# Performance work log

Measured on AMD Instinct MI355X. Metric: run time of the kernel, lower is better.

## Reference

```python
import jax, jax.numpy as jnp
import numpy as np

D = 64   # combine_doc_emb_len
H = 2    # heads
B = 256
S = 1024
SIDE = 56  # uid 32 + os 8 + zip 16

def _prelu(x, a):
    return jnp.where(x >= 0, x, a * x)

def _l2norm(x):
    n = jnp.sqrt(jnp.sum(x * x, axis=-1, keepdims=True))
    return x / jnp.maximum(n, 1e-12)

def _attn_branch(x_trans, y_trans, side, w1, b1, a1, w2, b2):
    b, s = x_trans.shape[0], x_trans.shape[1]
    xh = x_trans.reshape(b, s, H, D).transpose(0, 2, 1, 3)   # [B,H,S,D]
    yh = y_trans.reshape(b, 1, H, D).transpose(0, 2, 1, 3)   # [B,H,1,D]
    yhb = jnp.broadcast_to(yh, (b, H, s, D))
    sideb = jnp.broadcast_to(side[:, None, None, :], (b, H, s, side.shape[-1]))
    feat = jnp.concatenate([xh, xh * yhb, xh - yhb, yhb, sideb], axis=-1)  # [B,H,S,4D+SIDE]
    h1 = _prelu(feat @ w1 + b1, a1)          # [B,H,S,40]
    p = (h1 @ w2 + b2)[..., 0]               # [B,H,S]
    out = jnp.einsum('bhsd,bhs->bhd', xh, p).reshape(b, H * D)
    return p, out

def setup_inputs():
    key = jax.random.key(0)
    k = jax.random.split(key, 20)
    def n(i, shape, sc=1.0):
        return sc * jax.random.normal(k[i], shape, dtype=jnp.float32)
    return {
        'local_x_embs': n(0, (B, S, D)),
        'nonlocal_x_embs': n(1, (B, S, D)),
        'y_embs': n(2, (B, D)),
        'user_id_embs': n(3, (B, 32)),
        'os_embs': n(4, (B, 8)),
        'zip_code_embs': n(5, (B, 16)),
        'w_ty': n(6, (D, H * D), 0.05), 'b_ty': n(7, (H * D,), 0.05), 'a_ty': jnp.float32(0.25),
        'w_lx': n(8, (D, H * D), 0.05), 'b_lx': n(9, (H * D,), 0.05), 'a_lx': jnp.float32(0.25),
        'w_nx': n(10, (D, H * D), 0.05), 'b_nx': n(11, (H * D,), 0.05), 'a_nx': jnp.float32(0.25),
        'lw1': n(12, (4 * D + SIDE, 40), 0.05), 'lb1': n(13, (40,), 0.05), 'la1': jnp.float32(0.25),
        'lw2': n(14, (40, 1), 0.05), 'lb2': n(15, (1,), 0.05),
        'nw1': n(16, (4 * D + SIDE, 40), 0.05), 'nb1': n(17, (40,), 0.05), 'na1': jnp.float32(0.25),
        'nw2': n(18, (40, 1), 0.05), 'nb2': n(19, (1,), 0.05),
    }

def reference(local_x_embs, nonlocal_x_embs, y_embs, user_id_embs, os_embs, zip_code_embs, w_ty, b_ty, a_ty, w_lx, b_lx, a_lx, w_nx, b_nx, a_nx, lw1, lb1, la1, lw2, lb2, nw1, nb1, na1, nw2, nb2):
    side = jnp.concatenate([user_id_embs, os_embs, zip_code_embs], axis=-1)  # [B,56]
    local_x_trans = _l2norm(_prelu(local_x_embs @ w_lx + b_lx, a_lx))        # [B,S,H*D]
    nonlocal_x_trans = _l2norm(_prelu(nonlocal_x_embs @ w_nx + b_nx, a_nx))
    y_trans = _l2norm(_prelu(y_embs @ w_ty + b_ty, a_ty))                    # [B,H*D]
    _, local_embs = _attn_branch(local_x_trans, y_trans, side, lw1, lb1, la1, lw2, lb2)
    _, nonlocal_embs = _attn_branch(nonlocal_x_trans, y_trans, side, nw1, nb1, na1, nw2, nb2)
    return (local_embs, nonlocal_embs)
```

## Files before the change

kernel.cpp:

```cpp
#include <hip/hip_runtime.h>

typedef unsigned short u16;
typedef unsigned int   u32;
typedef __attribute__((ext_vector_type(8))) short bf8_t;
typedef __attribute__((ext_vector_type(4))) float f4_t;

#define NB 256
#define NS 1024

__device__ __forceinline__ u16 f2bf(float f){
    u32 u = __float_as_uint(f);
    return (u16)((u + 0x7fffu + ((u >> 16) & 1u)) >> 16);
}
__device__ __forceinline__ u32 pack_trunc(float lo, float hi){
    return __builtin_amdgcn_perm(__float_as_uint(hi), __float_as_uint(lo), 0x07060302u);
}

__global__ __launch_bounds__(256) void prep_kernel(
    const float* __restrict__ y,    const float* __restrict__ wty,
    const float* __restrict__ bty,  const float* __restrict__ aty,
    const float* __restrict__ uid,  const float* __restrict__ ose, const float* __restrict__ zipc,
    const float* __restrict__ wlx,  const float* __restrict__ wnx,
    const float* __restrict__ lw1,  const float* __restrict__ lb1,
    const float* __restrict__ nw1,  const float* __restrict__ nb1,
    u32* __restrict__ wtf, u32* __restrict__ weff, float* __restrict__ cs)
{
    const int tid = threadIdx.x;
    const int bx  = blockIdx.x;

    if (bx >= 512) {
        int u = (bx - 512)*256 + tid;
        int lane = u & 63, fr = u >> 6;
        int br = fr >> 4, t = fr & 15, n = t >> 1, ks = t & 1;
        int q = lane >> 4, lm = lane & 15;
        const float* W = br ? wnx : wlx;
        u32 out[4];
        #pragma unroll
        for (int p = 0; p < 4; ++p) {
            int k = ks*32 + q*8 + p*2;
            float lo = W[k*128 + n*16 + lm];
            float hi = W[(k+1)*128 + n*16 + lm];
            out[p] = (u32)f2bf(lo) | ((u32)f2bf(hi) << 16);
        }
        *(uint4*)&wtf[u*4] = make_uint4(out[0], out[1], out[2], out[3]);
        return;
    }

    __shared__ float yl[64];
    __shared__ float sq[128];
    __shared__ float yv[128];
    __shared__ float cpart[240];

    const int b  = bx >> 1;
    const int br = bx & 1;
    const float* w1 = br ? nw1 : lw1;
    const float* b1 = br ? nb1 : lb1;

    if (tid < 64) yl[tid] = y[b*64 + tid];
    __syncthreads();
    float v = 0.f;
    if (tid < 128) {
        float acc = bty[tid];
        for (int k = 0; k < 64; ++k) acc = fmaf(yl[k], wty[k*128 + tid], acc);
        float a = aty[0];
        v = (acc >= 0.f) ? acc : a * acc;
        sq[tid] = v * v;
    }
    __syncthreads();
    for (int s = 64; s >= 1; s >>= 1) { if (tid < s) sq[tid] += sq[tid+s]; __syncthreads(); }
    if (tid < 128) yv[tid] = v * (1.f / fmaxf(sqrtf(sq[0]), 1e-12f));
    __syncthreads();

    for (int u = tid; u < 768; u += 256) {
        int lane = u & 63, fr = u >> 6;
        int h = fr / 6, t = fr % 6, nj = t >> 1, ks = t & 1;
        int q = lane >> 4, lm = lane & 15, j = nj*16 + lm;
        u32 out[4];
        #pragma unroll
        for (int p = 0; p < 4; ++p) {
            u32 w = 0;
            #pragma unroll
            for (int e = 0; e < 2; ++e) {
                int k = ks*32 + q*8 + p*2 + e;
                float val = 0.f;
                if (j < 40)
                    val = w1[k*40 + j] + w1[(128+k)*40 + j] + yv[h*64 + k] * w1[(64+k)*40 + j];
                w |= ((u32)f2bf(val)) << (16*e);
            }
            out[p] = w;
        }
        *(uint4*)&weff[((size_t)(br*NB + b)*12 + fr)*64*4 + lane*4] =
            make_uint4(out[0], out[1], out[2], out[3]);
    }

    if (tid < 240) {
        int cj = tid / 3, sl = tid % 3;
        int h = cj / 40, j = cj % 40;
        float acc = 0.f;
        for (int t = sl*40; t < sl*40 + 40; ++t) {
            if (t < 64) {
                acc = fmaf(yv[h*64 + t], w1[(192+t)*40 + j] - w1[(128+t)*40 + j], acc);
            } else {
                int u = t - 64;
                float sv, wv;
                if (u < 32)      { sv = uid[b*32 + u];        wv = w1[(256+u)*40 + j]; }
                else if (u < 40) { sv = ose[b*8 + (u-32)];    wv = w1[(288+(u-32))*40 + j]; }
                else             { sv = zipc[b*16 + (u-40)];  wv = w1[(296+(u-40))*40 + j]; }
                acc = fmaf(sv, wv, acc);
            }
        }
        cpart[tid] = acc;
    }
    __syncthreads();
    if (tid < 96) {
        int h = tid / 48, jj = tid % 48;
        float val = 0.f;
        if (jj < 40) {
            int cj = h*40 + jj;
            val = b1[jj] + cpart[cj*3] + cpart[cj*3+1] + cpart[cj*3+2];
        }
        cs[(size_t)(br*NB + b)*96 + tid] = val;
    }
}

__global__ __launch_bounds__(512, 4) void main_kernel(
    const float* __restrict__ xloc, const float* __restrict__ xnon,
    const float* __restrict__ blx,  const float* __restrict__ alx,
    const float* __restrict__ bnx,  const float* __restrict__ anx,
    const float* __restrict__ la1,  const float* __restrict__ lw2, const float* __restrict__ lb2,
    const float* __restrict__ na1,  const float* __restrict__ nw2, const float* __restrict__ nb2,
    const u32* __restrict__ wtf, const u32* __restrict__ weff, const float* __restrict__ cs,
    float* __restrict__ out)
{
    __shared__ u16   tn[8*16*136];
    __shared__ u32   bf_sm[4096];
    __shared__ u32   cf_sm[3072];
    __shared__ float bias_sm[128];
    __shared__ float cs_sm[96];

    const int tid  = threadIdx.x;
    const int b    = blockIdx.x;
    const int br   = blockIdx.y;
    const int w    = tid >> 6;
    const int lane = tid & 63;
    const int q    = lane >> 4;
    const int lm   = lane & 15;

    const float* xg   = br ? xnon : xloc;
    const float* bias = br ? bnx  : blx;
    const float  am1  = (br ? anx[0] : alx[0]) - 1.f;
    const float  a1m1 = (br ? na1[0] : la1[0]) - 1.f;
    const float  b2v  = br ? nb2[0] : lb2[0];
    const float* w2   = br ? nw2  : lw2;

    {
        const uint4* wsrc = (const uint4*)wtf + br*1024;
        uint4* bdst = (uint4*)bf_sm;
        bdst[tid]       = wsrc[tid];
        bdst[512 + tid] = wsrc[512 + tid];
        const uint4* csrc = (const uint4*)weff + (size_t)(br*NB + b)*768;
        uint4* cdst = (uint4*)cf_sm;
        cdst[tid] = csrc[tid];
        if (tid < 256) cdst[512 + tid] = csrc[512 + tid];
    }
    if (tid < 128) bias_sm[tid] = bias[tid];
    if (tid < 96)  cs_sm[tid]   = cs[(size_t)(br*NB + b)*96 + tid];

    float w2v[3][4];
    #pragma unroll
    for (int nj = 0; nj < 3; ++nj)
        #pragma unroll
        for (int r = 0; r < 4; ++r) {
            int j = nj*16 + q*4 + r;
            w2v[nj][r] = (j < 40) ? w2[j] : 0.f;
        }

    __syncthreads();

    u16* tw = &tn[w*2176];
    const f4_t zero4 = {0.f, 0.f, 0.f, 0.f};
    float outp[8][4];
    #pragma unroll
    for (int c = 0; c < 8; ++c)
        #pragma unroll
        for (int r = 0; r < 4; ++r) outp[c][r] = 0.f;

    const float* xb = &xg[(size_t)b*NS*64];

    float4 p0, p1, p2, p3;
    {
        const float* xr = xb + (size_t)(w*16 + lm)*64;
        p0 = *(const float4*)(xr + q*8);
        p1 = *(const float4*)(xr + q*8 + 4);
        p2 = *(const float4*)(xr + 32 + q*8);
        p3 = *(const float4*)(xr + 32 + q*8 + 4);
    }

    #pragma unroll 1
    for (int it = 0; it < 8; ++it) {
        u32 zoff = 0;
        asm volatile("" : "+v"(zoff));
        const u32*   bfp = bf_sm + zoff;
        const u32*   cfp = cf_sm + zoff;
        const float* bip = bias_sm + zoff;
        const float* cvp = cs_sm + zoff;

        float4 c0 = p0, c1 = p1, c2 = p2, c3 = p3;
        if (it < 7) {
            const float* xr = xb + (size_t)(((it+1)*8 + w)*16 + lm)*64;
            p0 = *(const float4*)(xr + q*8);
            p1 = *(const float4*)(xr + q*8 + 4);
            p2 = *(const float4*)(xr + 32 + q*8);
            p3 = *(const float4*)(xr + 32 + q*8 + 4);
        }
        union { u32 u[4]; bf8_t v; } A0, A1;
        A0.u[0] = pack_trunc(c0.x, c0.y); A0.u[1] = pack_trunc(c0.z, c0.w);
        A0.u[2] = pack_trunc(c1.x, c1.y); A0.u[3] = pack_trunc(c1.z, c1.w);
        A1.u[0] = pack_trunc(c2.x, c2.y); A1.u[1] = pack_trunc(c2.z, c2.w);
        A1.u[2] = pack_trunc(c3.x, c3.y); A1.u[3] = pack_trunc(c3.z, c3.w);

        float tv[8][4];
        float s0 = 0.f, s1 = 0.f, s2 = 0.f, s3 = 0.f;
        #pragma unroll
        for (int c = 0; c < 8; ++c) {
            f4_t bi = *(const f4_t*)&bip[c*16 + q*4];
            bf8_t bf0 = *(const bf8_t*)&bfp[((c*2 + 0)*64 + lane)*4];
            bf8_t bf1 = *(const bf8_t*)&bfp[((c*2 + 1)*64 + lane)*4];
            f4_t acc = __builtin_amdgcn_mfma_f32_16x16x32_bf16(bf0, A0.v, bi,  0, 0, 0);
            acc      = __builtin_amdgcn_mfma_f32_16x16x32_bf16(bf1, A1.v, acc, 0, 0, 0);
            float v0 = acc[0]; v0 = fmaf(fminf(v0, 0.f), am1, v0); tv[c][0] = v0; s0 = fmaf(v0, v0, s0);
            float v1 = acc[1]; v1 = fmaf(fminf(v1, 0.f), am1, v1); tv[c][1] = v1; s1 = fmaf(v1, v1, s1);
            float v2 = acc[2]; v2 = fmaf(fminf(v2, 0.f), am1, v2); tv[c][2] = v2; s2 = fmaf(v2, v2, s2);
            float v3 = acc[3]; v3 = fmaf(fminf(v3, 0.f), am1, v3); tv[c][3] = v3; s3 = fmaf(v3, v3, s3);
        }
        float ssq = (s0 + s1) + (s2 + s3);
        ssq += __shfl_xor(ssq, 16);
        ssq += __shfl_xor(ssq, 32);
        const float rinv = 1.f / fmaxf(sqrtf(ssq), 1e-12f);

        #pragma unroll
        for (int c = 0; c < 8; ++c) {
            u32 lo = pack_trunc(tv[c][0], tv[c][1]);
            u32 hi = pack_trunc(tv[c][2], tv[c][3]);
            *(uint2*)&tw[lm*136 + c*16 + q*4] = make_uint2(lo, hi);
        }

        float pw[2];
        #pragma unroll
        for (int h = 0; h < 2; ++h) {
            bf8_t ac0 = *(const bf8_t*)&tw[lm*136 + h*64 + q*8];
            bf8_t ac1 = *(const bf8_t*)&tw[lm*136 + h*64 + 32 + q*8];
            float pp[3];
            #pragma unroll
            for (int nj = 0; nj < 3; ++nj) {
                f4_t cv = *(const f4_t*)&cvp[h*48 + nj*16 + q*4];
                bf8_t cf0 = *(const bf8_t*)&cfp[((h*6 + nj*2 + 0)*64 + lane)*4];
                bf8_t cf1 = *(const bf8_t*)&cfp[((h*6 + nj*2 + 1)*64 + lane)*4];
                f4_t acc = __builtin_amdgcn_mfma_f32_16x16x32_bf16(cf0, ac0, zero4, 0, 0, 0);
                acc      = __builtin_amdgcn_mfma_f32_16x16x32_bf16(cf1, ac1, acc,   0, 0, 0);
                float ppl = 0.f;
                #pragma unroll
                for (int r = 0; r < 4; ++r) {
                    float vv = fmaf(acc[r], rinv, cv[r]);
                    vv = fmaf(fminf(vv, 0.f), a1m1, vv);
                    ppl = fmaf(vv, w2v[nj][r], ppl);
                }
                pp[nj] = ppl;
            }
            float p = (pp[0] + pp[1]) + pp[2];
            p += __shfl_xor(p, 16);
            p += __shfl_xor(p, 32);
            pw[h] = (p + b2v) * rinv;
        }

        #pragma unroll
        for (int c = 0; c < 8; ++c)
            #pragma unroll
            for (int r = 0; r < 4; ++r)
                outp[c][r] = fmaf(tv[c][r], pw[c >> 2], outp[c][r]);
    }

    #pragma unroll
    for (int c = 0; c < 8; ++c)
        #pragma unroll
        for (int r = 0; r < 4; ++r) {
            float v = outp[c][r];
            v += __shfl_xor(v, 1);
            v += __shfl_xor(v, 2);
            v += __shfl_xor(v, 4);
            v += __shfl_xor(v, 8);
            outp[c][r] = v;
        }

    __syncthreads();
    float* red = (float*)tn;
    if (lm == 0) {
        #pragma unroll
        for (int c = 0; c < 8; ++c) {
            f4_t v = { outp[c][0], outp[c][1], outp[c][2], outp[c][3] };
            *(f4_t*)&red[w*128 + c*16 + q*4] = v;
        }
    }
    __syncthreads();
    if (tid < 128) {
        float s = 0.f;
        #pragma unroll
        for (int ww = 0; ww < 8; ++ww) s += red[ww*128 + tid];
        out[((size_t)br*NB + b)*128 + tid] = s;
    }
}

extern "C" void kernel_launch(void* const* d_in, const int* in_sizes, int n_in,
                              void* d_out, int out_size, void* d_ws, size_t ws_size,
                              hipStream_t stream)
{
    const float* xl  = (const float*)d_in[0];
    const float* xn  = (const float*)d_in[1];
    const float* y   = (const float*)d_in[2];
    const float* uid = (const float*)d_in[3];
    const float* ose = (const float*)d_in[4];
    const float* zp  = (const float*)d_in[5];
    const float* wty = (const float*)d_in[6];
    const float* bty = (const float*)d_in[7];
    const float* aty = (const float*)d_in[8];
    const float* wlx = (const float*)d_in[9];
    const float* blx = (const float*)d_in[10];
    const float* alx = (const float*)d_in[11];
    const float* wnx = (const float*)d_in[12];
    const float* bnx = (const float*)d_in[13];
    const float* anx = (const float*)d_in[14];
    const float* lw1 = (const float*)d_in[15];
    const float* lb1 = (const float*)d_in[16];
    const float* la1 = (const float*)d_in[17];
    const float* lw2 = (const float*)d_in[18];
    const float* lb2 = (const float*)d_in[19];
    const float* nw1 = (const float*)d_in[20];
    const float* nb1 = (const float*)d_in[21];
    const float* na1 = (const float*)d_in[22];
    const float* nw2 = (const float*)d_in[23];
    const float* nb2 = (const float*)d_in[24];

    u32*   wtf  = (u32*)d_ws;
    u32*   weff = (u32*)((char*)d_ws + 32768);
    float* cs   = (float*)((char*)d_ws + 32768 + 6291456);

    prep_kernel<<<dim3(520), dim3(256), 0, stream>>>(
        y, wty, bty, aty, uid, ose, zp, wlx, wnx, lw1, lb1, nw1, nb1, wtf, weff, cs);
    main_kernel<<<dim3(NB, 2), dim3(512), 0, stream>>>(
        xl, xn, blx, alx, bnx, anx,
        la1, lw2, lb2, na1, nw2, nb2,
        wtf, weff, cs, (float*)d_out);
}
```

Measured before the change: 273.8 us.

## Split sequence across two blocks per batch with atomic output accumulation

The main kernel now launches 256-thread blocks over a 3D grid, so each (batch, branch) pair is split into two blocks that each handle half of the sequence. Partial results are combined with atomicAdd into an output zeroed by a memset. The w2 weights move from registers into shared memory, and the register-level prefetch of the next x tile is dropped. This aims for more blocks and better occupancy and load balance across CUs, at the cost of a memset, atomics, loading the per-block weights into LDS twice, and losing the load/compute overlap.

```diff
diff --git a/kernel.cpp b/kernel.cpp
--- a/kernel.cpp
+++ b/kernel.cpp
@@ -123,7 +123,7 @@
     }
 }
 
-__global__ __launch_bounds__(512, 4) void main_kernel(
+__global__ __launch_bounds__(256, 2) void main_kernel(
     const float* __restrict__ xloc, const float* __restrict__ xnon,
     const float* __restrict__ blx,  const float* __restrict__ alx,
     const float* __restrict__ bnx,  const float* __restrict__ anx,
@@ -132,15 +132,17 @@
     const u32* __restrict__ wtf, const u32* __restrict__ weff, const float* __restrict__ cs,
     float* __restrict__ out)
 {
-    __shared__ u16   tn[8*16*136];
+    __shared__ u16   tn[4*16*136];
     __shared__ u32   bf_sm[4096];
     __shared__ u32   cf_sm[3072];
     __shared__ float bias_sm[128];
     __shared__ float cs_sm[96];
+    __shared__ float w2_sm[48];
 
     const int tid  = threadIdx.x;
     const int b    = blockIdx.x;
     const int br   = blockIdx.y;
+    const int zc   = blockIdx.z;
     const int w    = tid >> 6;
     const int lane = tid & 63;
     const int q    = lane >> 4;
@@ -156,24 +158,16 @@
     {
         const uint4* wsrc = (const uint4*)wtf + br*1024;
         uint4* bdst = (uint4*)bf_sm;
-        bdst[tid]       = wsrc[tid];
-        bdst[512 + tid] = wsrc[512 + tid];
+        #pragma unroll
+        for (int k = 0; k < 4; ++k) bdst[k*256 + tid] = wsrc[k*256 + tid];
         const uint4* csrc = (const uint4*)weff + (size_t)(br*NB + b)*768;
         uint4* cdst = (uint4*)cf_sm;
-        cdst[tid] = csrc[tid];
-        if (tid < 256) cdst[512 + tid] = csrc[512 + tid];
+        #pragma unroll
+        for (int k = 0; k < 3; ++k) cdst[k*256 + tid] = csrc[k*256 + tid];
     }
     if (tid < 128) bias_sm[tid] = bias[tid];
     if (tid < 96)  cs_sm[tid]   = cs[(size_t)(br*NB + b)*96 + tid];
-
-    float w2v[3][4];
-    #pragma unroll
-    for (int nj = 0; nj < 3; ++nj)
-        #pragma unroll
-        for (int r = 0; r < 4; ++r) {
-            int j = nj*16 + q*4 + r;
-            w2v[nj][r] = (j < 40) ? w2[j] : 0.f;
-        }
+    if (tid < 48)  w2_sm[tid]   = (tid < 40) ? w2[tid] : 0.f;
 
     __syncthreads();
 
@@ -186,15 +180,6 @@
         for (int r = 0; r < 4; ++r) outp[c][r] = 0.f;
 
     const float* xb = &xg[(size_t)b*NS*64];
-
-    float4 p0, p1, p2, p3;
-    {
-        const float* xr = xb + (size_t)(w*16 + lm)*64;
-        p0 = *(const float4*)(xr + q*8);
-        p1 = *(const float4*)(xr + q*8 + 4);
-        p2 = *(const float4*)(xr + 32 + q*8);
-        p3 = *(const float4*)(xr + 32 + q*8 + 4);
-    }
 
     #pragma unroll 1
     for (int it = 0; it < 8; ++it) {
@@ -204,15 +189,14 @@
         const u32*   cfp = cf_sm + zoff;
         const float* bip = bias_sm + zoff;
         const float* cvp = cs_sm + zoff;
-
-        float4 c0 = p0, c1 = p1, c2 = p2, c3 = p3;
-        if (it < 7) {
-            const float* xr = xb + (size_t)(((it+1)*8 + w)*16 + lm)*64;
-            p0 = *(const float4*)(xr + q*8);
-            p1 = *(const float4*)(xr + q*8 + 4);
-            p2 = *(const float4*)(xr + 32 + q*8);
-            p3 = *(const float4*)(xr + 32 + q*8 + 4);
-        }
+        const float* w2p = w2_sm + zoff;
+
+        const float* xr = xb + (size_t)((zc*32 + it*4 + w)*16 + lm)*64;
+        float4 c0 = *(const float4*)(xr + q*8);
+        float4 c1 = *(const float4*)(xr + q*8 + 4);
+        float4 c2 = *(const float4*)(xr + 32 + q*8);
+        float4 c3 = *(const float4*)(xr + 32 + q*8 + 4);
+
         union { u32 u[4]; bf8_t v; } A0, A1;
         A0.u[0] = pack_trunc(c0.x, c0.y); A0.u[1] = pack_trunc(c0.z, c0.w);
         A0.u[2] = pack_trunc(c1.x, c1.y); A0.u[3] = pack_trunc(c1.z, c1.w);
@@ -254,6 +238,7 @@
             #pragma unroll
             for (int nj = 0; nj < 3; ++nj) {
                 f4_t cv = *(const f4_t*)&cvp[h*48 + nj*16 + q*4];
+                f4_t wv = *(const f4_t*)&w2p[nj*16 + q*4];
                 bf8_t cf0 = *(const bf8_t*)&cfp[((h*6 + nj*2 + 0)*64 + lane)*4];
                 bf8_t cf1 = *(const bf8_t*)&cfp[((h*6 + nj*2 + 1)*64 + lane)*4];
                 f4_t acc = __builtin_amdgcn_mfma_f32_16x16x32_bf16(cf0, ac0, zero4, 0, 0, 0);
@@ -263,7 +248,7 @@
                 for (int r = 0; r < 4; ++r) {
                     float vv = fmaf(acc[r], rinv, cv[r]);
                     vv = fmaf(fminf(vv, 0.f), a1m1, vv);
-                    ppl = fmaf(vv, w2v[nj][r], ppl);
+                    ppl = fmaf(vv, wv[r], ppl);
                 }
                 pp[nj] = ppl;
             }
@@ -303,10 +288,8 @@
     }
     __syncthreads();
     if (tid < 128) {
-        float s = 0.f;
-        #pragma unroll
-        for (int ww = 0; ww < 8; ++ww) s += red[ww*128 + tid];
-        out[((size_t)br*NB + b)*128 + tid] = s;
+        float s = red[tid] + red[128 + tid] + red[256 + tid] + red[384 + tid];
+        atomicAdd(&out[((size_t)br*NB + b)*128 + tid], s);
     }
 }
 
@@ -344,9 +327,10 @@
     u32*   weff = (u32*)((char*)d_ws + 32768);
     float* cs   = (float*)((char*)d_ws + 32768 + 6291456);
 
+    hipMemsetAsync(d_out, 0, (size_t)out_size * sizeof(float), stream);
     prep_kernel<<<dim3(520), dim3(256), 0, stream>>>(
         y, wty, bty, aty, uid, ose, zp, wlx, wnx, lw1, lb1, nw1, nb1, wtf, weff, cs);
-    main_kernel<<<dim3(NB, 2), dim3(512), 0, stream>>>(
+    main_kernel<<<dim3(NB, 2, 2), dim3(256), 0, stream>>>(
         xl, xn, blx, alx, bnx, anx,
         la1, lw2, lb2, na1, nw2, nb2,
         wtf, weff, cs, (float*)d_out);
```

Result: faster. 247.9 us (-9.4%).
